# Performance work log

Hardware: AMD Instinct MI355X
Metric: run time of the kernel (lower is better)

## Reference

```python
import jax, jax.numpy as jnp
import numpy as np
from jax import lax

WINDOW_SIZE = 11
SIGMA = 1.5
C1 = 0.01 ** 2
C2 = 0.03 ** 2


def _create_window(window_size, channel):
    xs = np.arange(window_size)
    g = np.exp(-((xs - window_size // 2) ** 2) / (2.0 * SIGMA ** 2))
    g = (g / g.sum()).astype(np.float32)
    w2d = np.outer(g, g)  # [k, k]
    # depthwise kernel in OIHW with feature_group_count=channel: [channel, 1, k, k]
    return jnp.asarray(np.broadcast_to(w2d, (channel, 1, window_size, window_size)).copy())


def _dw_conv(x, window, pad):
    # x: [B, C, H, W], window: [C, 1, k, k]; depthwise conv, SAME-style padding
    c = x.shape[1]
    return lax.conv_general_dilated(
        x, window,
        window_strides=(1, 1),
        padding=[(pad, pad), (pad, pad)],
        dimension_numbers=('NCHW', 'OIHW', 'NCHW'),
        feature_group_count=c,
    )


def setup_inputs() -> dict:
    key = jax.random.key(0)
    k1, k2 = jax.random.split(key)
    img1 = jax.random.uniform(k1, (32, 1, 512, 512), dtype=jnp.float32)
    img2 = jax.random.uniform(k2, (32, 1, 512, 512), dtype=jnp.float32)
    return {"img1": img1, "img2": img2}


def reference(img1, img2):
    channel = img1.shape[1]
    pad = WINDOW_SIZE // 2
    window = _create_window(WINDOW_SIZE, channel)

    mu1 = _dw_conv(img1, window, pad)
    mu2 = _dw_conv(img2, window, pad)
    mu1_sq = mu1 * mu1
    mu2_sq = mu2 * mu2
    mu1_mu2 = mu1 * mu2

    sigma1_sq = _dw_conv(img1 * img1, window, pad) - mu1_sq
    sigma2_sq = _dw_conv(img2 * img2, window, pad) - mu2_sq
    sigma12 = _dw_conv(img1 * img2, window, pad) - mu1_mu2

    ssim_map = ((2.0 * mu1_mu2 + C1) * (2.0 * sigma12 + C2)) / (
        (mu1_sq + mu2_sq + C1) * (sigma1_sq + sigma2_sq + C2))
    return 1.0 - jnp.mean(ssim_map)
```

## Files before the change

kernel.cpp:

```cpp
#include <hip/hip_runtime.h>

typedef _Float16 f16x8 __attribute__((ext_vector_type(8)));
typedef _Float16 f16x4 __attribute__((ext_vector_type(4)));
typedef __fp16 fp16x2 __attribute__((ext_vector_type(2)));
typedef float f32x4 __attribute__((ext_vector_type(4)));

#define IMG 512
#define NB 32
#define OUTC 118
#define OUTR 32
#define GX 5
#define GY 16
#define NBLK (GX*GY*NB)
#define INSTR 48
#define IOFF (128*INSTR)
#define VSTR 136
#define VOFF (16*VSTR)
#define VLEN (5*VOFF + 32)
#define BUF0 (2*IOFF)

#define GW_LIST { 0.0010283804f, 0.0075987583f, 0.0360007700f, 0.1093606900f, \
  0.2130055300f, 0.2660117200f, 0.2130055300f, 0.1093606900f, 0.0360007700f, \
  0.0075987583f, 0.0010283804f }

__global__ __launch_bounds__(256, 3) void ssim_mfma(const float* __restrict__ img1,
                                                    const float* __restrict__ img2,
                                                    float* __restrict__ partials) {
    __shared__ _Float16 smem[BUF0 + VLEN];
    __shared__ _Float16 gwt[64];
    __shared__ float red[4];

    const int tid  = threadIdx.x;
    const int lane = tid & 63;
    const int lm   = lane & 15;
    const int kg   = lane >> 4;
    const int w    = tid >> 6;

    const int bx = blockIdx.x, by = blockIdx.y, bz = blockIdx.z;
    const float* __restrict__ p1 = img1 + (size_t)bz * (IMG*IMG);
    const float* __restrict__ p2 = img2 + (size_t)bz * (IMG*IMG);
    const int x0 = bx * OUTC;
    const int y0 = by * OUTR;

    const int ci = tid & 127;
    const int hh = tid >> 7;
    const int gc = x0 - 5 + ci;
    const bool okc = (gc >= 0) && (gc < IMG);
    const int gcc  = okc ? gc : 0;

    {
        union { fp16x2 p2v[12]; f16x8 v[3]; } ua, ub;
        const int slot0 = hh * 24;
#pragma unroll
        for (int pp = 0; pp < 12; ++pp) {
            const int s0 = slot0 + 2*pp;
            const int ar0 = y0 - 5 + s0;
            const int ar1 = ar0 + 1;
            const bool ok0 = okc & (s0   < 42) & (ar0 >= 0) & (ar0 < IMG);
            const bool ok1 = okc & (s0+1 < 42) & (ar1 >= 0) & (ar1 < IMG);
            const int i0 = ok0 ? ar0 : 0, i1 = ok1 ? ar1 : 0;
            float a0 = p1[i0*IMG + gcc], a1 = p1[i1*IMG + gcc];
            float b0 = p2[i0*IMG + gcc], b1 = p2[i1*IMG + gcc];
            a0 = ok0 ? a0 : 0.f;  a1 = ok1 ? a1 : 0.f;
            b0 = ok0 ? b0 : 0.f;  b1 = ok1 ? b1 : 0.f;
            ua.p2v[pp] = __builtin_amdgcn_cvt_pkrtz(a0, a1);
            ub.p2v[pp] = __builtin_amdgcn_cvt_pkrtz(b0, b1);
        }
        _Float16* dst = &smem[ci*INSTR + slot0];
#pragma unroll
        for (int m = 0; m < 3; ++m) {
            *(f16x8*)(dst + 8*m)        = ua.v[m];
            *(f16x8*)(dst + IOFF + 8*m) = ub.v[m];
        }
    }
    {
        const float GWc[11] = GW_LIST;
        if (tid < 64) {
            float wv = 0.f;
            const int t = tid - 16;
#pragma unroll
            for (int k = 0; k < 11; ++k) if (t == k) wv = GWc[k];
            gwt[tid] = (_Float16)wv;
        }
        f16x8 z = {};
        if (tid >= 64 && tid < 144) {
            const int u = tid - 64;
            const int f = u / 16, r = u % 16;
            *(f16x8*)&smem[BUF0 + f*VOFF + r*VSTR + 128] = z;
        } else if (tid >= 144 && tid < 148) {
            *(f16x8*)&smem[BUF0 + 5*VOFF + (tid-144)*8] = z;
        }
    }
    __syncthreads();

    union { _Float16 h[8]; f16x8 v; } wu;
#pragma unroll
    for (int i = 0; i < 8; ++i) wu.h[i] = gwt[16 + kg*8 + i - lm];

    const f32x4 zc = {0.f, 0.f, 0.f, 0.f};

    f16x4 pk[2][2][5];
#pragma unroll
    for (int s = 0; s < 2; ++s) {
#pragma unroll
        for (int q = 0; q < 2; ++q) {
            const int cb = 2*w + q;
            const _Float16* colp = &smem[(cb*16 + lm)*INSTR + s*16 + kg*8];
            const f16x8 xf = *(const f16x8*)colp;
            const f16x8 yf = *(const f16x8*)(colp + IOFF);
            const f16x8 fr[5] = { xf, yf, xf*xf, yf*yf, xf*yf };
#pragma unroll
            for (int f = 0; f < 5; ++f) {
                const f32x4 d = __builtin_amdgcn_mfma_f32_16x16x32_f16(fr[f], wu.v, zc, 0, 0, 0);
                union { fp16x2 p[2]; f16x4 v4; } c;
                c.p[0] = __builtin_amdgcn_cvt_pkrtz(d[0], d[1]);
                c.p[1] = __builtin_amdgcn_cvt_pkrtz(d[2], d[3]);
                pk[s][q][f] = c.v4;
            }
        }
    }

    {
        _Float16* b = &smem[BUF0 + lm*VSTR + 2*w*16 + kg*4];
#pragma unroll
        for (int q = 0; q < 2; ++q)
#pragma unroll
            for (int f = 0; f < 5; ++f)
                *(f16x4*)(b + f*VOFF + q*16) = pk[0][q][f];
    }
    __syncthreads();

    {
        _Float16* b = &smem[lm*VSTR + 2*w*16 + kg*4];
#pragma unroll
        for (int q = 0; q < 2; ++q)
#pragma unroll
            for (int f = 0; f < 5; ++f)
                *(f16x4*)(b + f*VOFF + q*16) = pk[1][q][f];
    }

    float local = 0.f;
    auto stage_h = [&](int base) {
#pragma unroll
        for (int q = 0; q < 2; ++q) {
            const int xx = 2*w + q;
            const _Float16* vp = &smem[base + lm*VSTR + xx*16 + kg*8];
            f32x4 d[5];
#pragma unroll
            for (int f = 0; f < 5; ++f) {
                const f16x8 a = *(const f16x8*)(vp + f*VOFF);
                d[f] = __builtin_amdgcn_mfma_f32_16x16x32_f16(a, wu.v, zc, 0, 0, 0);
            }
            const int X = xx*16 + lm;
            const bool valid = (X < OUTC) & (x0 + X < IMG);
            float s4 = 0.f;
#pragma unroll
            for (int j = 0; j < 4; ++j) {
                const float mu1 = d[0][j], mu2 = d[1][j];
                const float m11 = mu1*mu1, m22 = mu2*mu2, m12 = mu1*mu2;
                const float s1 = d[2][j] - m11, s2 = d[3][j] - m22, sx = d[4][j] - m12;
                const float num = (2.f*m12 + 1e-4f) * (2.f*sx + 9e-4f);
                const float den = (m11 + m22 + 1e-4f) * (s1 + s2 + 9e-4f);
                s4 += num * __builtin_amdgcn_rcpf(den);
            }
            local += valid ? s4 : 0.f;
        }
    };

    stage_h(BUF0);
    __syncthreads();
    stage_h(0);

#pragma unroll
    for (int off = 32; off > 0; off >>= 1)
        local += __shfl_down(local, off, 64);
    if (lane == 0) red[w] = local;
    __syncthreads();
    if (tid == 0) {
        partials[(size_t)((bz*GY + by)*GX + bx)] = red[0] + red[1] + red[2] + red[3];
    }
}

__global__ __launch_bounds__(256) void ssim_finalize(const float* __restrict__ partials,
                                                     float* __restrict__ out) {
    __shared__ double red[4];
    double s = 0.0;
    for (int i = threadIdx.x; i < NBLK/4; i += 256) {
        const float4 v = reinterpret_cast<const float4*>(partials)[i];
        s += (double)v.x + (double)v.y + (double)v.z + (double)v.w;
    }
#pragma unroll
    for (int off = 32; off > 0; off >>= 1)
        s += __shfl_down(s, off, 64);
    if ((threadIdx.x & 63) == 0) red[threadIdx.x >> 6] = s;
    __syncthreads();
    if (threadIdx.x == 0) {
        double tot = red[0] + red[1] + red[2] + red[3];
        out[0] = (float)(1.0 - tot / (32.0 * 512.0 * 512.0));
    }
}

extern "C" void kernel_launch(void* const* d_in, const int* in_sizes, int n_in,
                              void* d_out, int out_size, void* d_ws, size_t ws_size,
                              hipStream_t stream) {
    const float* img1 = (const float*)d_in[0];
    const float* img2 = (const float*)d_in[1];
    float* out = (float*)d_out;
    float* partials = (float*)d_ws;

    dim3 grid(GX, GY, NB);
    ssim_mfma<<<grid, 256, 0, stream>>>(img1, img2, partials);
    ssim_finalize<<<1, 256, 0, stream>>>(partials, out);
}
```

Measured before the change: 28.25 us.

## Make each wave stage its own columns, build weights in registers, swizzle blocks

Each wave now loads exactly the 32 input columns it later consumes in the vertical MFMA pass. That lets the block-wide barrier between the global load and the first MFMA stage be removed and replaced by per-wave LDS ordering. The Gaussian weight fragment is built in registers with ds_bpermute instead of going through a shared-memory table, and the zero-padding stores move to after the first stage. Block indices are remapped with an interleave by 8, likely to spread neighbouring tiles across XCDs and caches. The risk is correctness if any cross-wave LDS dependency was missed, plus a few extra integer ops for the index remap.

Result: faster. 25.81 us (-8.6%).

```diff
diff --git a/kernel.cpp b/kernel.cpp
--- a/kernel.cpp
+++ b/kernel.cpp
@@ -27,7 +27,6 @@
                                                     const float* __restrict__ img2,
                                                     float* __restrict__ partials) {
     __shared__ _Float16 smem[BUF0 + VLEN];
-    __shared__ _Float16 gwt[64];
     __shared__ float red[4];
 
     const int tid  = threadIdx.x;
@@ -36,21 +35,47 @@
     const int kg   = lane >> 4;
     const int w    = tid >> 6;
 
-    const int bx = blockIdx.x, by = blockIdx.y, bz = blockIdx.z;
+    const int d   = (blockIdx.z * GY + blockIdx.y) * GX + blockIdx.x;
+    const int wid = (d & 7) * (NBLK / 8) + (d >> 3);
+    const int bx  = wid % GX;
+    const int t2  = wid / GX;
+    const int by  = t2 % GY;
+    const int bz  = t2 / GY;
+
     const float* __restrict__ p1 = img1 + (size_t)bz * (IMG*IMG);
     const float* __restrict__ p2 = img2 + (size_t)bz * (IMG*IMG);
     const int x0 = bx * OUTC;
     const int y0 = by * OUTR;
 
-    const int ci = tid & 127;
-    const int hh = tid >> 7;
-    const int gc = x0 - 5 + ci;
-    const bool okc = (gc >= 0) && (gc < IMG);
-    const int gcc  = okc ? gc : 0;
-
-    {
+    union { fp16x2 p[4]; f16x8 v; } wu;
+    {
+        const float GWc[11] = GW_LIST;
+        float gf = 0.f;
+#pragma unroll
+        for (int k = 0; k < 11; ++k) gf = (lane == k) ? GWc[k] : gf;
+        const int gi = __float_as_int(gf);
+        float hv[8];
+#pragma unroll
+        for (int i = 0; i < 8; ++i) {
+            const int t = kg*8 + i - lm;
+            const int bp = __builtin_amdgcn_ds_bpermute(t * 4, gi);
+            hv[i] = ((unsigned)t < 11u) ? __int_as_float(bp) : 0.f;
+        }
+#pragma unroll
+        for (int j = 0; j < 4; ++j)
+            wu.p[j] = __builtin_amdgcn_cvt_pkrtz(hv[2*j], hv[2*j+1]);
+    }
+
+    {
+        const int cl   = lane & 31;
+        const int half = lane >> 5;
+        const int ci   = w*32 + cl;
+        const int gc   = x0 - 5 + ci;
+        const bool okc = (gc >= 0) && (gc < IMG);
+        const int gcc  = okc ? gc : 0;
+        const int slot0 = half * 24;
+
         union { fp16x2 p2v[12]; f16x8 v[3]; } ua, ub;
-        const int slot0 = hh * 24;
 #pragma unroll
         for (int pp = 0; pp < 12; ++pp) {
             const int s0 = slot0 + 2*pp;
@@ -73,29 +98,6 @@
             *(f16x8*)(dst + IOFF + 8*m) = ub.v[m];
         }
     }
-    {
-        const float GWc[11] = GW_LIST;
-        if (tid < 64) {
-            float wv = 0.f;
-            const int t = tid - 16;
-#pragma unroll
-            for (int k = 0; k < 11; ++k) if (t == k) wv = GWc[k];
-            gwt[tid] = (_Float16)wv;
-        }
-        f16x8 z = {};
-        if (tid >= 64 && tid < 144) {
-            const int u = tid - 64;
-            const int f = u / 16, r = u % 16;
-            *(f16x8*)&smem[BUF0 + f*VOFF + r*VSTR + 128] = z;
-        } else if (tid >= 144 && tid < 148) {
-            *(f16x8*)&smem[BUF0 + 5*VOFF + (tid-144)*8] = z;
-        }
-    }
-    __syncthreads();
-
-    union { _Float16 h[8]; f16x8 v; } wu;
-#pragma unroll
-    for (int i = 0; i < 8; ++i) wu.h[i] = gwt[16 + kg*8 + i - lm];
 
     const f32x4 zc = {0.f, 0.f, 0.f, 0.f};
 
@@ -111,10 +113,10 @@
             const f16x8 fr[5] = { xf, yf, xf*xf, yf*yf, xf*yf };
 #pragma unroll
             for (int f = 0; f < 5; ++f) {
-                const f32x4 d = __builtin_amdgcn_mfma_f32_16x16x32_f16(fr[f], wu.v, zc, 0, 0, 0);
+                const f32x4 dd = __builtin_amdgcn_mfma_f32_16x16x32_f16(fr[f], wu.v, zc, 0, 0, 0);
                 union { fp16x2 p[2]; f16x4 v4; } c;
-                c.p[0] = __builtin_amdgcn_cvt_pkrtz(d[0], d[1]);
-                c.p[1] = __builtin_amdgcn_cvt_pkrtz(d[2], d[3]);
+                c.p[0] = __builtin_amdgcn_cvt_pkrtz(dd[0], dd[1]);
+                c.p[1] = __builtin_amdgcn_cvt_pkrtz(dd[2], dd[3]);
                 pk[s][q][f] = c.v4;
             }
         }
@@ -127,6 +129,14 @@
 #pragma unroll
             for (int f = 0; f < 5; ++f)
                 *(f16x4*)(b + f*VOFF + q*16) = pk[0][q][f];
+
+        f16x8 z = {};
+        if (tid < 80) {
+            const int f = tid / 16, r = tid % 16;
+            *(f16x8*)&smem[BUF0 + f*VOFF + r*VSTR + 128] = z;
+        } else if (tid < 84) {
+            *(f16x8*)&smem[BUF0 + 5*VOFF + (tid-80)*8] = z;
+        }
     }
     __syncthreads();
 
@@ -145,20 +155,20 @@
         for (int q = 0; q < 2; ++q) {
             const int xx = 2*w + q;
             const _Float16* vp = &smem[base + lm*VSTR + xx*16 + kg*8];
-            f32x4 d[5];
+            f32x4 dd[5];
 #pragma unroll
             for (int f = 0; f < 5; ++f) {
                 const f16x8 a = *(const f16x8*)(vp + f*VOFF);
-                d[f] = __builtin_amdgcn_mfma_f32_16x16x32_f16(a, wu.v, zc, 0, 0, 0);
+                dd[f] = __builtin_amdgcn_mfma_f32_16x16x32_f16(a, wu.v, zc, 0, 0, 0);
             }
             const int X = xx*16 + lm;
             const bool valid = (X < OUTC) & (x0 + X < IMG);
             float s4 = 0.f;
 #pragma unroll
             for (int j = 0; j < 4; ++j) {
-                const float mu1 = d[0][j], mu2 = d[1][j];
+                const float mu1 = dd[0][j], mu2 = dd[1][j];
                 const float m11 = mu1*mu1, m22 = mu2*mu2, m12 = mu1*mu2;
-                const float s1 = d[2][j] - m11, s2 = d[3][j] - m22, sx = d[4][j] - m12;
+                const float s1 = dd[2][j] - m11, s2 = dd[3][j] - m22, sx = dd[4][j] - m12;
                 const float num = (2.f*m12 + 1e-4f) * (2.f*sx + 9e-4f);
                 const float den = (m11 + m22 + 1e-4f) * (s1 + s2 + 9e-4f);
                 s4 += num * __builtin_amdgcn_rcpf(den);
@@ -177,7 +187,7 @@
     if (lane == 0) red[w] = local;
     __syncthreads();
     if (tid == 0) {
-        partials[(size_t)((bz*GY + by)*GX + bx)] = red[0] + red[1] + red[2] + red[3];
+        partials[(size_t)wid] = red[0] + red[1] + red[2] + red[3];
     }
 }
 
```
